# Optimization experiments

Hardware: AMD Instinct MI355X
Metric: run time of the kernel (lower is better)

The kernel has to match this reference:

```python
import jax, jax.numpy as jnp
import numpy as np

N_NODES = 25000
N_EDGES = 300000
B = 25            # graphs in the batch
NPG = N_NODES // B
D = 128           # hidden_dim == out_dim
H = 8             # num_heads
HD = D // H
L = 4             # num_layers
VOCAB = 30000
N_ETYPE = 8


def setup_inputs() -> dict:
    key = jax.random.key(0)
    ks = jax.random.split(key, 16)
    s = 0.05
    # graph structure: edges kept within each graph
    eg = jax.random.randint(ks[0], (N_EDGES,), 0, B)
    src = eg * NPG + jax.random.randint(ks[1], (N_EDGES,), 0, NPG)
    dst = eg * NPG + jax.random.randint(ks[2], (N_EDGES,), 0, NPG)
    tokens = jax.random.randint(ks[3], (N_NODES,), 0, VOCAB)
    etype = jax.random.randint(ks[4], (N_EDGES,), 0, N_ETYPE)
    graph_id = jnp.arange(N_NODES) // NPG
    return {
        "emb_h": jax.random.normal(ks[5], (VOCAB, D)) * s,
        "emb_e": jax.random.normal(ks[6], (N_ETYPE, D)) * s,
        # per-layer stacked params: Q,K,V,proj_e weights (bias=False)
        "w_qkve": jax.random.normal(ks[7], (L, 4, D, D)) * s,
        # output projections O_h, O_e
        "o_w": jax.random.normal(ks[8], (L, 2, D, D)) * s,
        "o_b": jnp.zeros((L, 2, D)),
        # layernorms: [ln1_h, ln1_e, ln2_h, ln2_e]
        "ln_scale": jnp.ones((L, 4, D)),
        "ln_bias": jnp.zeros((L, 4, D)),
        # FFNs for h and e: D -> 2D -> D
        "ffn_w1": jax.random.normal(ks[9], (L, 2, D, 2 * D)) * s,
        "ffn_b1": jnp.zeros((L, 2, 2 * D)),
        "ffn_w2": jax.random.normal(ks[10], (L, 2, 2 * D, D)) * s,
        "ffn_b2": jnp.zeros((L, 2, D)),
        # MLPReadout (L=2): 128 -> 64 -> 32 -> 1
        "mlp_w0": jax.random.normal(ks[11], (D, D // 2)) * s,
        "mlp_b0": jnp.zeros((D // 2,)),
        "mlp_w1": jax.random.normal(ks[12], (D // 2, D // 4)) * s,
        "mlp_b1": jnp.zeros((D // 4,)),
        "mlp_w2": jax.random.normal(ks[13], (D // 4, 1)) * s,
        "mlp_b2": jnp.zeros((1,)),
        "tokens": tokens,
        "etype": etype,
        "src": src,
        "dst": dst,
        "graph_id": graph_id,
    }


def _ln(x, g, b):
    m = jnp.mean(x, axis=-1, keepdims=True)
    v = jnp.mean(jnp.square(x - m), axis=-1, keepdims=True)
    return g * (x - m) / jnp.sqrt(v + 1e-5) + b


def _layer(h, e, src, dst, wq, wk, wv, we, o_w, o_b, ln_s, ln_b,
           ffn_w1, ffn_b1, ffn_w2, ffn_b2):
    n = h.shape[0]
    Q = (h @ wq).reshape(n, H, HD)
    K = (h @ wk).reshape(n, H, HD)
    V = (h @ wv).reshape(n, H, HD)
    pe = (e @ we).reshape(-1, H, HD)
    # per-edge implicit attention: (K_src * Q_dst)/sqrt(d) * proj_e
    score = (K[src] * Q[dst]) / jnp.sqrt(jnp.asarray(HD, h.dtype)) * pe  # [E,H,HD]
    e_att = score.reshape(-1, D)
    w = jnp.exp(jnp.clip(jnp.sum(score, axis=-1, keepdims=True), -5.0, 5.0))  # [E,H,1]
    wV = jax.ops.segment_sum((V[src] * w).reshape(-1, D), dst, num_segments=n)
    z = jax.ops.segment_sum(w[:, :, 0], dst, num_segments=n)  # [N,H]
    h_att = (wV.reshape(n, H, HD) / (z[:, :, None] + 1e-6)).reshape(n, D)
    # O proj + residual + LN
    h1 = _ln(h + (h_att @ o_w[0] + o_b[0]), ln_s[0], ln_b[0])
    e1 = _ln(e + (e_att @ o_w[1] + o_b[1]), ln_s[1], ln_b[1])
    # FFNs + residual + LN
    h2 = _ln(h1 + jax.nn.relu(h1 @ ffn_w1[0] + ffn_b1[0]) @ ffn_w2[0] + ffn_b2[0],
             ln_s[2], ln_b[2])
    e2 = _ln(e1 + jax.nn.relu(e1 @ ffn_w1[1] + ffn_b1[1]) @ ffn_w2[1] + ffn_b2[1],
             ln_s[3], ln_b[3])
    return h2, e2


def reference(emb_h, emb_e, w_qkve, o_w, o_b, ln_scale, ln_bias,
              ffn_w1, ffn_b1, ffn_w2, ffn_b2,
              mlp_w0, mlp_b0, mlp_w1, mlp_b1, mlp_w2, mlp_b2,
              tokens, etype, src, dst, graph_id):
    h = emb_h[tokens]   # [N,D]
    e = emb_e[etype]    # [E,D]
    for l in range(L):
        h, e = _layer(h, e, src, dst,
                      w_qkve[l, 0], w_qkve[l, 1], w_qkve[l, 2], w_qkve[l, 3],
                      o_w[l], o_b[l], ln_scale[l], ln_bias[l],
                      ffn_w1[l], ffn_b1[l], ffn_w2[l], ffn_b2[l])
    # mean-nodes readout per graph
    hg_sum = jax.ops.segment_sum(h, graph_id, num_segments=B)
    cnt = jax.ops.segment_sum(jnp.ones((h.shape[0], 1), h.dtype), graph_id, num_segments=B)
    hg = hg_sum / cnt
    # MLPReadout
    y = jax.nn.relu(hg @ mlp_w0 + mlp_b0)
    y = jax.nn.relu(y @ mlp_w1 + mlp_b1)
    return y @ mlp_w2 + mlp_b2  # [B,1]
```

## Files before the change

### kernel.cpp

```cpp
#include <hip/hip_runtime.h>
#include <cstdint>

#define NN 25000
#define NE 300000

typedef unsigned short ushort_t;
typedef __attribute__((ext_vector_type(8))) short bf16x8;
typedef __attribute__((ext_vector_type(4))) float f32x4;
typedef __attribute__((ext_vector_type(4))) unsigned short u16x4;
typedef __attribute__((ext_vector_type(8))) unsigned short u16x8;

__device__ __forceinline__ float4 ld4(const float* p){ return *reinterpret_cast<const float4*>(p); }
__device__ __forceinline__ void st4(float* p, const float4& v){ *reinterpret_cast<float4*>(p) = v; }
__device__ __forceinline__ float bf2f(ushort_t u){ return __uint_as_float((unsigned)u << 16); }
__device__ __forceinline__ ushort_t f2bfu(float f){
  unsigned x = __float_as_uint(f);
  return (ushort_t)((x + 0x7fffu + ((x >> 16) & 1u)) >> 16);
}

#define FXS 4294967296.0
#define FXI 2.3283064365386963e-10
__device__ __forceinline__ long long f2fx(float v) {
  return (long long)llrint((double)v * FXS);
}
__device__ __forceinline__ float fx2f(long long q) { return (float)((double)q * FXI); }

#define MFMA(a, b, c) __builtin_amdgcn_mfma_f32_16x16x32_bf16((a), (b), (c), 0, 0, 0)

__global__ __launch_bounds__(256)
void wconv_k(const float* __restrict__ src, ushort_t* __restrict__ dst,
             int K, int N, int total)
{
  int i = blockIdx.x * 256 + threadIdx.x;
  if (i >= total) return;
  int kn = K * N;
  int mat = i / kn, r = i - mat * kn;
  int n = r / K, k = r - n * K;
  dst[i] = f2bfu(src[(size_t)mat * kn + (size_t)k * N + n]);
}

__global__ __launch_bounds__(256)
void gather_h_k(const float* __restrict__ tab, const int* __restrict__ idx,
                float* __restrict__ hf, ushort_t* __restrict__ hb)
{
  int t = blockIdx.x * 256 + threadIdx.x;
  if (t >= NN * 32) return;
  int i = t >> 5, c4 = t & 31;
  float4 v = ld4(tab + (size_t)idx[i] * 128 + c4 * 4);
  st4(hf + (size_t)i * 128 + c4 * 4, v);
  u16x4 b = { f2bfu(v.x), f2bfu(v.y), f2bfu(v.z), f2bfu(v.w) };
  *reinterpret_cast<u16x4*>(hb + (size_t)i * 128 + c4 * 4) = b;
}

__global__ __launch_bounds__(256)
void gather_e_k(const float* __restrict__ tab, const int* __restrict__ idx,
                ushort_t* __restrict__ eb)
{
  int t = blockIdx.x * 256 + threadIdx.x;
  if (t >= NE * 32) return;
  int i = t >> 5, c4 = t & 31;
  float4 v = ld4(tab + (size_t)idx[i] * 128 + c4 * 4);
  u16x4 b = { f2bfu(v.x), f2bfu(v.y), f2bfu(v.z), f2bfu(v.w) };
  *reinterpret_cast<u16x4*>(eb + (size_t)i * 128 + c4 * 4) = b;
}

__global__ __launch_bounds__(256)
void count_k(const int* __restrict__ dst, int* __restrict__ counts)
{
  int e = blockIdx.x * 256 + threadIdx.x;
  if (e < NE) atomicAdd(&counts[dst[e]], 1);
}

__global__ __launch_bounds__(1024)
void scan_k(const int* __restrict__ counts, int* __restrict__ start,
            int* __restrict__ cursor)
{
  __shared__ int part[1024];
  const int t = threadIdx.x;
  const int base = t * 25;
  int loc[25];
  int s = 0;
#pragma unroll
  for (int i = 0; i < 25; ++i) {
    int n = base + i;
    int c = (n < NN) ? counts[n] : 0;
    loc[i] = s; s += c;
  }
  part[t] = s;
  __syncthreads();
  for (int off = 1; off < 1024; off <<= 1) {
    int v = (t >= off) ? part[t - off] : 0;
    __syncthreads();
    part[t] += v;
    __syncthreads();
  }
  int excl = (t == 0) ? 0 : part[t - 1];
#pragma unroll
  for (int i = 0; i < 25; ++i) {
    int n = base + i;
    if (n < NN) { int v = excl + loc[i]; start[n] = v; cursor[n] = v; }
  }
  if (t == 0) start[NN] = NE;
}

__global__ __launch_bounds__(256)
void scatter_k(const int* __restrict__ src, const int* __restrict__ dst,
               int* __restrict__ cursor, int2* __restrict__ csr_es)
{
  int e = blockIdx.x * 256 + threadIdx.x;
  if (e >= NE) return;
  int pos = atomicAdd(&cursor[dst[e]], 1);
  csr_es[pos] = make_int2(e, src[e]);
}

__global__ __launch_bounds__(256)
void gemmN_bf_k(const ushort_t* __restrict__ A, const ushort_t* __restrict__ WT,
                const int K, const int M, const int ldo,
                const float* __restrict__ Bias, const int osep,
                const float* __restrict__ ResF, const ushort_t* __restrict__ ResB,
                const float* __restrict__ G, const float* __restrict__ Bb,
                ushort_t* __restrict__ OutB, float* __restrict__ OutF)
{
  __shared__ __align__(16) ushort_t SM[2 * 128 * 136];
  __shared__ float mu[128], rs[128];
  ushort_t* Xs = SM;
  ushort_t* Ws = SM + 128 * 136;
  const int tid = threadIdx.x;
  const int m0 = blockIdx.x * 128;
  const int col0 = blockIdx.y * 128;

  const int l = tid & 63, wv = tid >> 6;
  const int lr = l & 15, lk = l >> 4;
  const int mb = (wv & 1) * 64, nb = (wv >> 1) * 64;
  f32x4 acc[4][4];
  const f32x4 zf = {0.f, 0.f, 0.f, 0.f};
#pragma unroll
  for (int mi = 0; mi < 4; ++mi)
#pragma unroll
    for (int ni = 0; ni < 4; ++ni) acc[mi][ni] = zf;

  for (int kc = 0; kc < K; kc += 128) {
    if (kc) __syncthreads();
    for (int c = tid; c < 2048; c += 256) {
      int r = c >> 4, k8 = c & 15;
      bf16x8 v = {};
      if (m0 + r < M)
        v = *reinterpret_cast<const bf16x8*>(A + (size_t)(m0 + r) * K + kc + k8 * 8);
      *reinterpret_cast<bf16x8*>(Xs + r * 136 + k8 * 8) = v;
    }
    for (int c = tid; c < 2048; c += 256) {
      int r = c >> 4, k8 = c & 15;
      *reinterpret_cast<bf16x8*>(Ws + r * 136 + k8 * 8) =
          *reinterpret_cast<const bf16x8*>(WT + (size_t)(col0 + r) * K + kc + k8 * 8);
    }
    __syncthreads();
#pragma unroll
    for (int kt = 0; kt < 4; ++kt) {
      bf16x8 af[4], bw[4];
#pragma unroll
      for (int i = 0; i < 4; ++i)
        af[i] = *reinterpret_cast<const bf16x8*>(Xs + (mb + i * 16 + lr) * 136 + kt * 32 + lk * 8);
#pragma unroll
      for (int i = 0; i < 4; ++i)
        bw[i] = *reinterpret_cast<const bf16x8*>(Ws + (nb + i * 16 + lr) * 136 + kt * 32 + lk * 8);
#pragma unroll
      for (int mi = 0; mi < 4; ++mi)
#pragma unroll
        for (int ni = 0; ni < 4; ++ni)
          acc[mi][ni] = MFMA(af[mi], bw[ni], acc[mi][ni]);
    }
  }

  if (G == nullptr) {
    __syncthreads();
    ushort_t* Rb = SM;
#pragma unroll
    for (int mi = 0; mi < 4; ++mi)
#pragma unroll
      for (int rr = 0; rr < 4; ++rr) {
        int row = mb + mi * 16 + lk * 4 + rr;
#pragma unroll
        for (int ni = 0; ni < 4; ++ni) {
          int col = nb + ni * 16 + lr;
          float v = acc[mi][ni][rr];
          if (Bias) v = fmaxf(v + Bias[col0 + col], 0.f);
          Rb[row * 136 + col] = f2bfu(v);
        }
      }
    __syncthreads();
    ushort_t* ob = OutB + (osep ? (size_t)blockIdx.y * M * 128 : (size_t)col0);
    for (int c = tid; c < 2048; c += 256) {
      int r = c >> 4, k8 = c & 15;
      if (m0 + r < M)
        *reinterpret_cast<u16x8*>(ob + (size_t)(m0 + r) * ldo + k8 * 8) =
            *reinterpret_cast<u16x8*>(Rb + r * 136 + k8 * 8);
    }
    return;
  }

  __syncthreads();
  float* Tf = reinterpret_cast<float*>(SM);
#pragma unroll
  for (int mi = 0; mi < 4; ++mi)
#pragma unroll
    for (int rr = 0; rr < 4; ++rr) {
      int row = mb + mi * 16 + lk * 4 + rr;
      int grow = m0 + row;
#pragma unroll
      for (int ni = 0; ni < 4; ++ni) {
        int col = nb + ni * 16 + lr;
        float t = acc[mi][ni][rr] + Bias[col];
        if (grow < M)
          t += ResF ? ResF[(size_t)grow * 128 + col] : bf2f(ResB[(size_t)grow * 128 + col]);
        Tf[row * 132 + col] = t;
      }
    }
  __syncthreads();
  {
    int r = tid >> 1, jj = tid & 1;
    const float* tp = Tf + r * 132 + jj * 64;
    float s = 0.f;
    for (int c2 = 0; c2 < 64; ++c2) s += tp[c2];
    s += __shfl_xor(s, 1);
    float mean = s * (1.f / 128.f);
    float v = 0.f;
    for (int c2 = 0; c2 < 64; ++c2) { float d = tp[c2] - mean; v += d * d; }
    v += __shfl_xor(v, 1);
    if (jj == 0) { mu[r] = mean; rs[r] = 1.f / sqrtf(v * (1.f / 128.f) + 1e-5f); }
  }
  __syncthreads();
  for (int c = tid; c < 4096; c += 256) {
    int r = c >> 5, c4 = c & 31;
    int grow = m0 + r;
    if (grow >= M) continue;
    float4 t = ld4(Tf + r * 132 + c4 * 4);
    float4 gv = ld4(G + c4 * 4), bv = ld4(Bb + c4 * 4);
    float m = mu[r], ir = rs[r];
    float o0 = gv.x * (t.x - m) * ir + bv.x;
    float o1 = gv.y * (t.y - m) * ir + bv.y;
    float o2 = gv.z * (t.z - m) * ir + bv.z;
    float o3 = gv.w * (t.w - m) * ir + bv.w;
    u16x4 ub = { f2bfu(o0), f2bfu(o1), f2bfu(o2), f2bfu(o3) };
    *reinterpret_cast<u16x4*>(OutB + (size_t)grow * 128 + c4 * 4) = ub;
    if (OutF) st4(OutF + (size_t)grow * 128 + c4 * 4, make_float4(o0, o1, o2, o3));
  }
}

__global__ __launch_bounds__(256)
void ffn_f_k(const ushort_t* __restrict__ Xbf, const float* __restrict__ ResF,
             const ushort_t* __restrict__ W1T, const float* __restrict__ B1,
             const ushort_t* __restrict__ W2T, const float* __restrict__ B2,
             const float* __restrict__ G, const float* __restrict__ Bb,
             ushort_t* __restrict__ OutB, float* __restrict__ OutF, int M)
{
  __shared__ __align__(16) ushort_t SM[8704 + 8704 + 17408];
  __shared__ float mu[64], rs[64];
  ushort_t* Xs   = SM;
  ushort_t* Mid0 = SM + 8704;
  ushort_t* Wst  = SM + 17408;
  const int tid = threadIdx.x;
  const int m0 = blockIdx.x * 64;
  const int l = tid & 63, wv = tid >> 6, lr = l & 15, lk = l >> 4;
  const f32x4 zf = {0.f, 0.f, 0.f, 0.f};

  for (int c = tid; c < 1024; c += 256) {
    int r = c >> 4, k8 = c & 15;
    bf16x8 v = {};
    if (m0 + r < M) v = *reinterpret_cast<const bf16x8*>(Xbf + (size_t)(m0 + r) * 128 + k8 * 8);
    *reinterpret_cast<bf16x8*>(Xs + r * 136 + k8 * 8) = v;
  }
  for (int c = tid; c < 2048; c += 256) {
    int r = c >> 4, k8 = c & 15;
    *reinterpret_cast<bf16x8*>(Wst + r * 136 + k8 * 8) =
        *reinterpret_cast<const bf16x8*>(W1T + (size_t)r * 128 + k8 * 8);
  }
  __syncthreads();

  f32x4 acc2[8];
#pragma unroll
  for (int i = 0; i < 8; ++i) acc2[i] = zf;
  ushort_t rsv[8][4];

  {
    f32x4 a1[8];
#pragma unroll
    for (int i = 0; i < 8; ++i) a1[i] = zf;
#pragma unroll
    for (int kt = 0; kt < 4; ++kt) {
      bf16x8 af = *reinterpret_cast<const bf16x8*>(Xs + (wv * 16 + lr) * 136 + kt * 32 + lk * 8);
#pragma unroll
      for (int ni = 0; ni < 8; ++ni) {
        bf16x8 bw = *reinterpret_cast<const bf16x8*>(Wst + (ni * 16 + lr) * 136 + kt * 32 + lk * 8);
        a1[ni] = MFMA(af, bw, a1[ni]);
      }
    }
#pragma unroll
    for (int ni = 0; ni < 8; ++ni)
#pragma unroll
      for (int rr = 0; rr < 4; ++rr)
        Mid0[(wv * 16 + lk * 4 + rr) * 136 + ni * 16 + lr] =
            f2bfu(fmaxf(a1[ni][rr] + B1[ni * 16 + lr], 0.f));
  }
  __syncthreads();
  for (int c = tid; c < 2048; c += 256) {
    int r = c >> 4, k8 = c & 15;
    *reinterpret_cast<bf16x8*>(Wst + r * 136 + k8 * 8) =
        *reinterpret_cast<const bf16x8*>(W1T + (size_t)(128 + r) * 128 + k8 * 8);
  }
  __syncthreads();
  {
    f32x4 a1[8];
#pragma unroll
    for (int i = 0; i < 8; ++i) a1[i] = zf;
#pragma unroll
    for (int kt = 0; kt < 4; ++kt) {
      bf16x8 af = *reinterpret_cast<const bf16x8*>(Xs + (wv * 16 + lr) * 136 + kt * 32 + lk * 8);
#pragma unroll
      for (int ni = 0; ni < 8; ++ni) {
        bf16x8 bw = *reinterpret_cast<const bf16x8*>(Wst + (ni * 16 + lr) * 136 + kt * 32 + lk * 8);
        a1[ni] = MFMA(af, bw, a1[ni]);
      }
    }
    __syncthreads();
    if (!ResF) {
#pragma unroll
      for (int ni = 0; ni < 8; ++ni)
#pragma unroll
        for (int rr = 0; rr < 4; ++rr)
          rsv[ni][rr] = Xs[(wv * 16 + lk * 4 + rr) * 136 + ni * 16 + lr];
    }
#pragma unroll
    for (int ni = 0; ni < 8; ++ni)
#pragma unroll
      for (int rr = 0; rr < 4; ++rr)
        Xs[(wv * 16 + lk * 4 + rr) * 136 + ni * 16 + lr] =
            f2bfu(fmaxf(a1[ni][rr] + B1[128 + ni * 16 + lr], 0.f));
  }
  __syncthreads();
  for (int c = tid; c < 2048; c += 256) {
    int r = c >> 4, k8 = c & 15;
    *reinterpret_cast<bf16x8*>(Wst + r * 136 + k8 * 8) =
        *reinterpret_cast<const bf16x8*>(W2T + (size_t)r * 256 + k8 * 8);
  }
  __syncthreads();
#pragma unroll
  for (int kt = 0; kt < 4; ++kt) {
    bf16x8 af = *reinterpret_cast<const bf16x8*>(Mid0 + (wv * 16 + lr) * 136 + kt * 32 + lk * 8);
#pragma unroll
    for (int ni = 0; ni < 8; ++ni) {
      bf16x8 bw = *reinterpret_cast<const bf16x8*>(Wst + (ni * 16 + lr) * 136 + kt * 32 + lk * 8);
      acc2[ni] = MFMA(af, bw, acc2[ni]);
    }
  }
  __syncthreads();
  for (int c = tid; c < 2048; c += 256) {
    int r = c >> 4, k8 = c & 15;
    *reinterpret_cast<bf16x8*>(Wst + r * 136 + k8 * 8) =
        *reinterpret_cast<const bf16x8*>(W2T + (size_t)r * 256 + 128 + k8 * 8);
  }
  __syncthreads();
#pragma unroll
  for (int kt = 0; kt < 4; ++kt) {
    bf16x8 af = *reinterpret_cast<const bf16x8*>(Xs + (wv * 16 + lr) * 136 + kt * 32 + lk * 8);
#pragma unroll
    for (int ni = 0; ni < 8; ++ni) {
      bf16x8 bw = *reinterpret_cast<const bf16x8*>(Wst + (ni * 16 + lr) * 136 + kt * 32 + lk * 8);
      acc2[ni] = MFMA(af, bw, acc2[ni]);
    }
  }
  __syncthreads();
  float* Tf = reinterpret_cast<float*>(Wst);
#pragma unroll
  for (int ni = 0; ni < 8; ++ni)
#pragma unroll
    for (int rr = 0; rr < 4; ++rr) {
      int row = wv * 16 + lk * 4 + rr;
      int grow = m0 + row;
      int col = ni * 16 + lr;
      float t = acc2[ni][rr] + B2[col];
      if (ResF) { if (grow < M) t += ResF[(size_t)grow * 128 + col]; }
      else      t += bf2f(rsv[ni][rr]);
      Tf[row * 132 + col] = t;
    }
  __syncthreads();
  {
    int r = tid >> 2, jj = tid & 3;
    const float* tp = Tf + r * 132 + jj * 32;
    float s = 0.f;
    for (int c2 = 0; c2 < 32; ++c2) s += tp[c2];
    s += __shfl_xor(s, 1); s += __shfl_xor(s, 2);
    float mean = s * (1.f / 128.f);
    float v = 0.f;
    for (int c2 = 0; c2 < 32; ++c2) { float d = tp[c2] - mean; v += d * d; }
    v += __shfl_xor(v, 1); v += __shfl_xor(v, 2);
    if (jj == 0) { mu[r] = mean; rs[r] = 1.f / sqrtf(v * (1.f / 128.f) + 1e-5f); }
  }
  __syncthreads();
  for (int c = tid; c < 2048; c += 256) {
    int r = c >> 5, c4 = c & 31;
    int grow = m0 + r;
    if (grow >= M) continue;
    float4 t = ld4(Tf + r * 132 + c4 * 4);
    float4 gv = ld4(G + c4 * 4), bv = ld4(Bb + c4 * 4);
    float m = mu[r], ir = rs[r];
    float o0 = gv.x * (t.x - m) * ir + bv.x;
    float o1 = gv.y * (t.y - m) * ir + bv.y;
    float o2 = gv.z * (t.z - m) * ir + bv.z;
    float o3 = gv.w * (t.w - m) * ir + bv.w;
    u16x4 ub = { f2bfu(o0), f2bfu(o1), f2bfu(o2), f2bfu(o3) };
    *reinterpret_cast<u16x4*>(OutB + (size_t)grow * 128 + c4 * 4) = ub;
    if (OutF) st4(OutF + (size_t)grow * 128 + c4 * 4, make_float4(o0, o1, o2, o3));
  }
}

__global__ __launch_bounds__(256)
void edge_score_k(const ushort_t* __restrict__ Q, const ushort_t* __restrict__ K,
                  ushort_t* __restrict__ PE,
                  const int* __restrict__ src, const int* __restrict__ dst,
                  float* __restrict__ wbuf)
{
  int t = blockIdx.x * 256 + threadIdx.x;
  int e = t >> 4;
  if (e >= NE) return;
  int j = t & 15;
  int s = src[e], d = dst[e];
  u16x8 kv = *reinterpret_cast<const u16x8*>(K + (size_t)s * 128 + j * 8);
  u16x8 qv = *reinterpret_cast<const u16x8*>(Q + (size_t)d * 128 + j * 8);
  u16x8 pv = *reinterpret_cast<const u16x8*>(PE + (size_t)e * 128 + j * 8);
  float hsum = 0.f;
  u16x8 ob;
#pragma unroll
  for (int i = 0; i < 8; ++i) {
    float x = bf2f(kv[i]) * bf2f(qv[i]) * 0.25f * bf2f(pv[i]);
    hsum += x; ob[i] = f2bfu(x);
  }
  *reinterpret_cast<u16x8*>(PE + (size_t)e * 128 + j * 8) = ob;
  hsum += __shfl_xor(hsum, 1);
  float w = expf(fminf(fmaxf(hsum, -5.f), 5.f));
  if ((j & 1) == 0) wbuf[(size_t)e * 8 + (j >> 1)] = w;
}

__global__ __launch_bounds__(256)
void reduce_k(const ushort_t* __restrict__ V, const float* __restrict__ wbuf,
              const int* __restrict__ start, const int2* __restrict__ csr_es,
              ushort_t* __restrict__ out)
{
  int t = blockIdx.x * 256 + threadIdx.x;
  int n = t >> 4;
  if (n >= NN) return;
  int j = t & 15;
  int p0 = start[n], p1 = start[n + 1];
  long long acc[8] = {};
  long long zacc = 0;
  for (int p = p0; p < p1; ++p) {
    int2 es = csr_es[p];
    float w = wbuf[(size_t)es.x * 8 + (j >> 1)];
    u16x8 vv = *reinterpret_cast<const u16x8*>(V + (size_t)es.y * 128 + j * 8);
    zacc += f2fx(w);
#pragma unroll
    for (int i = 0; i < 8; ++i) acc[i] += f2fx(bf2f(vv[i]) * w);
  }
  float zz = fx2f(zacc) + 1e-6f;
  u16x8 ob;
#pragma unroll
  for (int i = 0; i < 8; ++i) ob[i] = f2bfu(fx2f(acc[i]) / zz);
  *reinterpret_cast<u16x8*>(out + (size_t)n * 128 + j * 8) = ob;
}

__global__ __launch_bounds__(256)
void graphmean_k(const float* __restrict__ h, float* __restrict__ hg)
{
  __shared__ float red[256];
  int g = blockIdx.x, tid = threadIdx.x;
  int c = tid & 127, half = tid >> 7;
  float s = 0.f;
  for (int r = half; r < 1000; r += 2) s += h[(size_t)(g * 1000 + r) * 128 + c];
  red[tid] = s;
  __syncthreads();
  if (half == 0) hg[g * 128 + c] = (red[c] + red[c + 128]) / 1000.0f;
}

__global__ __launch_bounds__(256)
void readout_k(const float* __restrict__ hg,
               const float* __restrict__ w0, const float* __restrict__ b0,
               const float* __restrict__ w1, const float* __restrict__ b1,
               const float* __restrict__ w2, const float* __restrict__ b2,
               float* __restrict__ out)
{
  __shared__ float hs[25 * 128];
  __shared__ float t0[25 * 64];
  __shared__ float t1[25 * 32];
  int tid = threadIdx.x;
  for (int i = tid; i < 25 * 128; i += 256) hs[i] = hg[i];
  __syncthreads();
  for (int i = tid; i < 25 * 64; i += 256) {
    int r = i >> 6, c = i & 63;
    float a = b0[c];
    for (int k = 0; k < 128; k++) a += hs[r * 128 + k] * w0[k * 64 + c];
    t0[i] = fmaxf(a, 0.f);
  }
  __syncthreads();
  for (int i = tid; i < 25 * 32; i += 256) {
    int r = i >> 5, c = i & 31;
    float a = b1[c];
    for (int k = 0; k < 64; k++) a += t0[r * 64 + k] * w1[k * 32 + c];
    t1[i] = fmaxf(a, 0.f);
  }
  __syncthreads();
  if (tid < 25) {
    float a = b2[0];
    for (int k = 0; k < 32; k++) a += t1[tid * 32 + k] * w2[k];
    out[tid] = a;
  }
}

extern "C" void kernel_launch(void* const* d_in, const int* in_sizes, int n_in,
                              void* d_out, int out_size, void* d_ws, size_t ws_size,
                              hipStream_t stream)
{
  const float* emb_h  = (const float*)d_in[0];
  const float* emb_e  = (const float*)d_in[1];
  const float* w_qkve = (const float*)d_in[2];
  const float* o_w    = (const float*)d_in[3];
  const float* o_b    = (const float*)d_in[4];
  const float* ln_s   = (const float*)d_in[5];
  const float* ln_b   = (const float*)d_in[6];
  const float* ffn_w1 = (const float*)d_in[7];
  const float* ffn_b1 = (const float*)d_in[8];
  const float* ffn_w2 = (const float*)d_in[9];
  const float* ffn_b2 = (const float*)d_in[10];
  const float* mlp_w0 = (const float*)d_in[11];
  const float* mlp_b0 = (const float*)d_in[12];
  const float* mlp_w1 = (const float*)d_in[13];
  const float* mlp_b1 = (const float*)d_in[14];
  const float* mlp_w2 = (const float*)d_in[15];
  const float* mlp_b2 = (const float*)d_in[16];
  const int* tokens = (const int*)d_in[17];
  const int* etype  = (const int*)d_in[18];
  const int* src    = (const int*)d_in[19];
  const int* dst    = (const int*)d_in[20];

  char* ws = (char*)d_ws;
  size_t off = 0;
  auto alloc = [&](size_t bytes) { char* p = ws + off; off += bytes; return p; };
  int2*      csr_es = (int2*)alloc((size_t)NE * 8);
  float*     h      = (float*)alloc((size_t)NN * 128 * 4);
  float*     hg     = (float*)alloc(25 * 128 * 4);
  float*     wbuf   = (float*)alloc((size_t)NE * 8 * 4);
  int*       counts = (int*)alloc((size_t)NN * 4);
  int*       cursor = (int*)alloc((size_t)NN * 4);
  int*       startp = (int*)alloc((size_t)(NN + 1) * 4);
  ushort_t*  h_bf   = (ushort_t*)alloc((size_t)NN * 128 * 2);
  ushort_t*  ha_bf  = (ushort_t*)alloc((size_t)NN * 128 * 2);
  ushort_t*  Qb     = (ushort_t*)alloc((size_t)NN * 128 * 2);
  ushort_t*  Kb     = (ushort_t*)alloc((size_t)NN * 128 * 2);
  ushort_t*  Vb     = (ushort_t*)alloc((size_t)NN * 128 * 2);
  ushort_t*  e_bf   = (ushort_t*)alloc((size_t)NE * 128 * 2);
  ushort_t*  sc_bf  = (ushort_t*)alloc((size_t)NE * 128 * 2);
  ushort_t*  wt     = (ushort_t*)alloc(917504 * 2);
  (void)Kb; (void)Vb;

  ushort_t* qkveT = wt;
  ushort_t* owT   = wt + 262144;
  ushort_t* w1T   = wt + 393216;
  ushort_t* w2T   = wt + 655360;
  wconv_k<<<1024, 256, 0, stream>>>(w_qkve, qkveT, 128, 128, 262144);
  wconv_k<<<512,  256, 0, stream>>>(o_w,    owT,   128, 128, 131072);
  wconv_k<<<1024, 256, 0, stream>>>(ffn_w1, w1T,   128, 256, 262144);
  wconv_k<<<1024, 256, 0, stream>>>(ffn_w2, w2T,   256, 128, 262144);

  gather_h_k<<<3125, 256, 0, stream>>>(emb_h, tokens, h, h_bf);
  gather_e_k<<<37500, 256, 0, stream>>>(emb_e, etype, e_bf);

  hipMemsetAsync(counts, 0, (size_t)NN * 4, stream);
  count_k<<<(NE + 255) / 256, 256, 0, stream>>>(dst, counts);
  scan_k<<<1, 1024, 0, stream>>>(counts, startp, cursor);
  scatter_k<<<(NE + 255) / 256, 256, 0, stream>>>(src, dst, cursor, csr_es);

  const int GN = (NN + 127) / 128;
  const int GE = (NE + 127) / 128;
  const int FN = (NN + 63) / 64;
  const int FE = (NE + 63) / 64;

  for (int l = 0; l < 4; ++l) {
    const ushort_t* qkvT = qkveT + (size_t)l * 4 * 16384;
    const ushort_t* weT  = qkveT + ((size_t)l * 4 + 3) * 16384;
    const ushort_t* ow0T = owT + ((size_t)l * 2 + 0) * 16384;
    const ushort_t* ow1T = owT + ((size_t)l * 2 + 1) * 16384;
    const ushort_t* w1hT = w1T + ((size_t)l * 2 + 0) * 32768;
    const ushort_t* w1eT = w1T + ((size_t)l * 2 + 1) * 32768;
    const ushort_t* w2hT = w2T + ((size_t)l * 2 + 0) * 32768;
    const ushort_t* w2eT = w2T + ((size_t)l * 2 + 1) * 32768;
    const float* ob0 = o_b + ((size_t)l * 2 + 0) * 128;
    const float* ob1 = o_b + ((size_t)l * 2 + 1) * 128;
    const float* ls0 = ln_s + ((size_t)l * 4 + 0) * 128;
    const float* ls1 = ln_s + ((size_t)l * 4 + 1) * 128;
    const float* ls2 = ln_s + ((size_t)l * 4 + 2) * 128;
    const float* ls3 = ln_s + ((size_t)l * 4 + 3) * 128;
    const float* lb0 = ln_b + ((size_t)l * 4 + 0) * 128;
    const float* lb1 = ln_b + ((size_t)l * 4 + 1) * 128;
    const float* lb2 = ln_b + ((size_t)l * 4 + 2) * 128;
    const float* lb3 = ln_b + ((size_t)l * 4 + 3) * 128;
    const float* fb1h = ffn_b1 + ((size_t)l * 2 + 0) * 256;
    const float* fb1e = ffn_b1 + ((size_t)l * 2 + 1) * 256;
    const float* fb2h = ffn_b2 + ((size_t)l * 2 + 0) * 128;
    const float* fb2e = ffn_b2 + ((size_t)l * 2 + 1) * 128;

    gemmN_bf_k<<<dim3(GN, 3), 256, 0, stream>>>(h_bf, qkvT, 128, NN, 128,
        nullptr, 1, nullptr, nullptr, nullptr, nullptr, Qb, nullptr);
    gemmN_bf_k<<<dim3(GE, 1), 256, 0, stream>>>(e_bf, weT, 128, NE, 128,
        nullptr, 0, nullptr, nullptr, nullptr, nullptr, sc_bf, nullptr);

    edge_score_k<<<18750, 256, 0, stream>>>(Qb, Kb, sc_bf, src, dst, wbuf);
    reduce_k<<<1563, 256, 0, stream>>>(Vb, wbuf, startp, csr_es, ha_bf);

    gemmN_bf_k<<<dim3(GN, 1), 256, 0, stream>>>(ha_bf, ow0T, 128, NN, 128,
        ob0, 0, h, nullptr, ls0, lb0, h_bf, h);
    gemmN_bf_k<<<dim3(GE, 1), 256, 0, stream>>>(sc_bf, ow1T, 128, NE, 128,
        ob1, 0, nullptr, e_bf, ls1, lb1, e_bf, nullptr);

    ffn_f_k<<<FN, 256, 0, stream>>>(h_bf, h, w1hT, fb1h, w2hT, fb2h,
                                    ls2, lb2, h_bf, h, NN);
    ffn_f_k<<<FE, 256, 0, stream>>>(e_bf, nullptr, w1eT, fb1e, w2eT, fb2e,
                                    ls3, lb3, e_bf, nullptr, NE);
  }

  graphmean_k<<<25, 256, 0, stream>>>(h, hg);
  readout_k<<<1, 256, 0, stream>>>(hg, mlp_w0, mlp_b0, mlp_w1, mlp_b1, mlp_w2, mlp_b2,
                                   (float*)d_out);
}
```

Baseline: 2.254 ms.

## Fuse edge projection, score, O_e projection, LN and edge FFN into one kernel

Replaces the per-layer edge pipeline (proj_e GEMM, edge score, O_e GEMM with residual+LN, edge FFN with LN) with a single kernel that keeps a 64-edge tile in shared memory across all stages. This removes several full round trips of the 300k x 128 bf16 edge tensor through global memory and the sc_bf scratch buffer. The cost is about 70KB of shared memory per block, which lowers occupancy, and many block-wide barriers with weights reloaded into shared memory for each stage.

```diff
diff --git a/kernel.cpp b/kernel.cpp
--- a/kernel.cpp
+++ b/kernel.cpp
@@ -414,30 +414,277 @@
 }
 
 __global__ __launch_bounds__(256)
-void edge_score_k(const ushort_t* __restrict__ Q, const ushort_t* __restrict__ K,
-                  ushort_t* __restrict__ PE,
-                  const int* __restrict__ src, const int* __restrict__ dst,
-                  float* __restrict__ wbuf)
-{
-  int t = blockIdx.x * 256 + threadIdx.x;
-  int e = t >> 4;
-  if (e >= NE) return;
-  int j = t & 15;
-  int s = src[e], d = dst[e];
-  u16x8 kv = *reinterpret_cast<const u16x8*>(K + (size_t)s * 128 + j * 8);
-  u16x8 qv = *reinterpret_cast<const u16x8*>(Q + (size_t)d * 128 + j * 8);
-  u16x8 pv = *reinterpret_cast<const u16x8*>(PE + (size_t)e * 128 + j * 8);
-  float hsum = 0.f;
-  u16x8 ob;
-#pragma unroll
-  for (int i = 0; i < 8; ++i) {
-    float x = bf2f(kv[i]) * bf2f(qv[i]) * 0.25f * bf2f(pv[i]);
-    hsum += x; ob[i] = f2bfu(x);
-  }
-  *reinterpret_cast<u16x8*>(PE + (size_t)e * 128 + j * 8) = ob;
-  hsum += __shfl_xor(hsum, 1);
-  float w = expf(fminf(fmaxf(hsum, -5.f), 5.f));
-  if ((j & 1) == 0) wbuf[(size_t)e * 8 + (j >> 1)] = w;
+void efused_k(ushort_t* __restrict__ Ebuf,
+              const ushort_t* __restrict__ Qb, const ushort_t* __restrict__ Kb,
+              const int* __restrict__ src, const int* __restrict__ dst,
+              float* __restrict__ wbuf,
+              const ushort_t* __restrict__ weT,
+              const ushort_t* __restrict__ owT, const float* __restrict__ oBias,
+              const float* __restrict__ G1, const float* __restrict__ B1n,
+              const ushort_t* __restrict__ W1T, const float* __restrict__ fB1,
+              const ushort_t* __restrict__ W2T, const float* __restrict__ fB2,
+              const float* __restrict__ G2, const float* __restrict__ B2n,
+              int M)
+{
+  __shared__ __align__(16) ushort_t SM[34816];
+  __shared__ float mu[64], rs[64];
+  ushort_t* Es   = SM;
+  ushort_t* Mid0 = SM + 8704;
+  ushort_t* Wst  = SM + 17408;
+  const int tid = threadIdx.x;
+  const int m0 = blockIdx.x * 64;
+  const int l = tid & 63, wv = tid >> 6, lr = l & 15, lk = l >> 4;
+  const f32x4 zf = {0.f, 0.f, 0.f, 0.f};
+
+  for (int c = tid; c < 1024; c += 256) {
+    int r = c >> 4, k8 = c & 15;
+    bf16x8 v = {};
+    if (m0 + r < M) v = *reinterpret_cast<const bf16x8*>(Ebuf + (size_t)(m0 + r) * 128 + k8 * 8);
+    *reinterpret_cast<bf16x8*>(Es + r * 136 + k8 * 8) = v;
+  }
+  for (int c = tid; c < 2048; c += 256) {
+    int r = c >> 4, k8 = c & 15;
+    *reinterpret_cast<bf16x8*>(Wst + r * 136 + k8 * 8) =
+        *reinterpret_cast<const bf16x8*>(weT + (size_t)r * 128 + k8 * 8);
+  }
+  __syncthreads();
+
+  {
+    f32x4 a1[8];
+#pragma unroll
+    for (int i = 0; i < 8; ++i) a1[i] = zf;
+#pragma unroll
+    for (int kt = 0; kt < 4; ++kt) {
+      bf16x8 af = *reinterpret_cast<const bf16x8*>(Es + (wv * 16 + lr) * 136 + kt * 32 + lk * 8);
+#pragma unroll
+      for (int ni = 0; ni < 8; ++ni) {
+        bf16x8 bw = *reinterpret_cast<const bf16x8*>(Wst + (ni * 16 + lr) * 136 + kt * 32 + lk * 8);
+        a1[ni] = MFMA(af, bw, a1[ni]);
+      }
+    }
+#pragma unroll
+    for (int ni = 0; ni < 8; ++ni)
+#pragma unroll
+      for (int rr = 0; rr < 4; ++rr)
+        Mid0[(wv * 16 + lk * 4 + rr) * 136 + ni * 16 + lr] = f2bfu(a1[ni][rr]);
+  }
+  __syncthreads();
+
+  for (int c = tid; c < 1024; c += 256) {
+    int r = c >> 4, j = c & 15;
+    int e = m0 + r;
+    if (e < M) {
+      int s = src[e], d = dst[e];
+      u16x8 kv = *reinterpret_cast<const u16x8*>(Kb + (size_t)s * 128 + j * 8);
+      u16x8 qv = *reinterpret_cast<const u16x8*>(Qb + (size_t)d * 128 + j * 8);
+      u16x8 pv = *reinterpret_cast<const u16x8*>(Mid0 + r * 136 + j * 8);
+      float hsum = 0.f;
+      u16x8 ob;
+#pragma unroll
+      for (int i = 0; i < 8; ++i) {
+        float x = bf2f(kv[i]) * bf2f(qv[i]) * 0.25f * bf2f(pv[i]);
+        hsum += x; ob[i] = f2bfu(x);
+      }
+      *reinterpret_cast<u16x8*>(Mid0 + r * 136 + j * 8) = ob;
+      hsum += __shfl_xor(hsum, 1);
+      float w = expf(fminf(fmaxf(hsum, -5.f), 5.f));
+      if ((j & 1) == 0) wbuf[(size_t)e * 8 + (j >> 1)] = w;
+    }
+  }
+  __syncthreads();
+
+  for (int c = tid; c < 2048; c += 256) {
+    int r = c >> 4, k8 = c & 15;
+    *reinterpret_cast<bf16x8*>(Wst + r * 136 + k8 * 8) =
+        *reinterpret_cast<const bf16x8*>(owT + (size_t)r * 128 + k8 * 8);
+  }
+  __syncthreads();
+
+  {
+    f32x4 a1[8];
+#pragma unroll
+    for (int i = 0; i < 8; ++i) a1[i] = zf;
+#pragma unroll
+    for (int kt = 0; kt < 4; ++kt) {
+      bf16x8 af = *reinterpret_cast<const bf16x8*>(Mid0 + (wv * 16 + lr) * 136 + kt * 32 + lk * 8);
+#pragma unroll
+      for (int ni = 0; ni < 8; ++ni) {
+        bf16x8 bw = *reinterpret_cast<const bf16x8*>(Wst + (ni * 16 + lr) * 136 + kt * 32 + lk * 8);
+        a1[ni] = MFMA(af, bw, a1[ni]);
+      }
+    }
+    __syncthreads();
+    float* Tf = reinterpret_cast<float*>(Wst);
+#pragma unroll
+    for (int ni = 0; ni < 8; ++ni)
+#pragma unroll
+      for (int rr = 0; rr < 4; ++rr) {
+        int row = wv * 16 + lk * 4 + rr;
+        int col = ni * 16 + lr;
+        Tf[row * 132 + col] = a1[ni][rr] + oBias[col] + bf2f(Es[row * 136 + col]);
+      }
+  }
+  __syncthreads();
+  {
+    float* Tf = reinterpret_cast<float*>(Wst);
+    int r = tid >> 2, jj = tid & 3;
+    const float* tp = Tf + r * 132 + jj * 32;
+    float s = 0.f;
+    for (int c2 = 0; c2 < 32; ++c2) s += tp[c2];
+    s += __shfl_xor(s, 1); s += __shfl_xor(s, 2);
+    float mean = s * (1.f / 128.f);
+    float v = 0.f;
+    for (int c2 = 0; c2 < 32; ++c2) { float d = tp[c2] - mean; v += d * d; }
+    v += __shfl_xor(v, 1); v += __shfl_xor(v, 2);
+    if (jj == 0) { mu[r] = mean; rs[r] = 1.f / sqrtf(v * (1.f / 128.f) + 1e-5f); }
+  }
+  __syncthreads();
+  {
+    float* Tf = reinterpret_cast<float*>(Wst);
+    for (int c = tid; c < 2048; c += 256) {
+      int r = c >> 5, c4 = c & 31;
+      float4 t = ld4(Tf + r * 132 + c4 * 4);
+      float4 gv = ld4(G1 + c4 * 4), bv = ld4(B1n + c4 * 4);
+      float m = mu[r], ir = rs[r];
+      u16x4 ub = { f2bfu(gv.x * (t.x - m) * ir + bv.x), f2bfu(gv.y * (t.y - m) * ir + bv.y),
+                   f2bfu(gv.z * (t.z - m) * ir + bv.z), f2bfu(gv.w * (t.w - m) * ir + bv.w) };
+      *reinterpret_cast<u16x4*>(Es + r * 136 + c4 * 4) = ub;
+    }
+  }
+  __syncthreads();
+
+  f32x4 acc2[8];
+#pragma unroll
+  for (int i = 0; i < 8; ++i) acc2[i] = zf;
+  ushort_t rsv[8][4];
+
+  for (int c = tid; c < 2048; c += 256) {
+    int r = c >> 4, k8 = c & 15;
+    *reinterpret_cast<bf16x8*>(Wst + r * 136 + k8 * 8) =
+        *reinterpret_cast<const bf16x8*>(W1T + (size_t)r * 128 + k8 * 8);
+  }
+  __syncthreads();
+  {
+    f32x4 a1[8];
+#pragma unroll
+    for (int i = 0; i < 8; ++i) a1[i] = zf;
+#pragma unroll
+    for (int kt = 0; kt < 4; ++kt) {
+      bf16x8 af = *reinterpret_cast<const bf16x8*>(Es + (wv * 16 + lr) * 136 + kt * 32 + lk * 8);
+#pragma unroll
+      for (int ni = 0; ni < 8; ++ni) {
+        bf16x8 bw = *reinterpret_cast<const bf16x8*>(Wst + (ni * 16 + lr) * 136 + kt * 32 + lk * 8);
+        a1[ni] = MFMA(af, bw, a1[ni]);
+      }
+    }
+    __syncthreads();
+#pragma unroll
+    for (int ni = 0; ni < 8; ++ni)
+#pragma unroll
+      for (int rr = 0; rr < 4; ++rr)
+        Mid0[(wv * 16 + lk * 4 + rr) * 136 + ni * 16 + lr] =
+            f2bfu(fmaxf(a1[ni][rr] + fB1[ni * 16 + lr], 0.f));
+  }
+  __syncthreads();
+  for (int c = tid; c < 2048; c += 256) {
+    int r = c >> 4, k8 = c & 15;
+    *reinterpret_cast<bf16x8*>(Wst + r * 136 + k8 * 8) =
+        *reinterpret_cast<const bf16x8*>(W1T + (size_t)(128 + r) * 128 + k8 * 8);
+  }
+  __syncthreads();
+  {
+    f32x4 a1[8];
+#pragma unroll
+    for (int i = 0; i < 8; ++i) a1[i] = zf;
+#pragma unroll
+    for (int kt = 0; kt < 4; ++kt) {
+      bf16x8 af = *reinterpret_cast<const bf16x8*>(Es + (wv * 16 + lr) * 136 + kt * 32 + lk * 8);
+#pragma unroll
+      for (int ni = 0; ni < 8; ++ni) {
+        bf16x8 bw = *reinterpret_cast<const bf16x8*>(Wst + (ni * 16 + lr) * 136 + kt * 32 + lk * 8);
+        a1[ni] = MFMA(af, bw, a1[ni]);
+      }
+    }
+    __syncthreads();
+#pragma unroll
+    for (int ni = 0; ni < 8; ++ni)
+#pragma unroll
+      for (int rr = 0; rr < 4; ++rr)
+        rsv[ni][rr] = Es[(wv * 16 + lk * 4 + rr) * 136 + ni * 16 + lr];
+#pragma unroll
+    for (int ni = 0; ni < 8; ++ni)
+#pragma unroll
+      for (int rr = 0; rr < 4; ++rr)
+        Es[(wv * 16 + lk * 4 + rr) * 136 + ni * 16 + lr] =
+            f2bfu(fmaxf(a1[ni][rr] + fB1[128 + ni * 16 + lr], 0.f));
+  }
+  __syncthreads();
+  for (int c = tid; c < 2048; c += 256) {
+    int r = c >> 4, k8 = c & 15;
+    *reinterpret_cast<bf16x8*>(Wst + r * 136 + k8 * 8) =
+        *reinterpret_cast<const bf16x8*>(W2T + (size_t)r * 256 + k8 * 8);
+  }
+  __syncthreads();
+#pragma unroll
+  for (int kt = 0; kt < 4; ++kt) {
+    bf16x8 af = *reinterpret_cast<const bf16x8*>(Mid0 + (wv * 16 + lr) * 136 + kt * 32 + lk * 8);
+#pragma unroll
+    for (int ni = 0; ni < 8; ++ni) {
+      bf16x8 bw = *reinterpret_cast<const bf16x8*>(Wst + (ni * 16 + lr) * 136 + kt * 32 + lk * 8);
+      acc2[ni] = MFMA(af, bw, acc2[ni]);
+    }
+  }
+  __syncthreads();
+  for (int c = tid; c < 2048; c += 256) {
+    int r = c >> 4, k8 = c & 15;
+    *reinterpret_cast<bf16x8*>(Wst + r * 136 + k8 * 8) =
+        *reinterpret_cast<const bf16x8*>(W2T + (size_t)r * 256 + 128 + k8 * 8);
+  }
+  __syncthreads();
+#pragma unroll
+  for (int kt = 0; kt < 4; ++kt) {
+    bf16x8 af = *reinterpret_cast<const bf16x8*>(Es + (wv * 16 + lr) * 136 + kt * 32 + lk * 8);
+#pragma unroll
+    for (int ni = 0; ni < 8; ++ni) {
+      bf16x8 bw = *reinterpret_cast<const bf16x8*>(Wst + (ni * 16 + lr) * 136 + kt * 32 + lk * 8);
+      acc2[ni] = MFMA(af, bw, acc2[ni]);
+    }
+  }
+  __syncthreads();
+  float* Tf = reinterpret_cast<float*>(Wst);
+#pragma unroll
+  for (int ni = 0; ni < 8; ++ni)
+#pragma unroll
+    for (int rr = 0; rr < 4; ++rr) {
+      int row = wv * 16 + lk * 4 + rr;
+      int col = ni * 16 + lr;
+      Tf[row * 132 + col] = acc2[ni][rr] + fB2[col] + bf2f(rsv[ni][rr]);
+    }
+  __syncthreads();
+  {
+    int r = tid >> 2, jj = tid & 3;
+    const float* tp = Tf + r * 132 + jj * 32;
+    float s = 0.f;
+    for (int c2 = 0; c2 < 32; ++c2) s += tp[c2];
+    s += __shfl_xor(s, 1); s += __shfl_xor(s, 2);
+    float mean = s * (1.f / 128.f);
+    float v = 0.f;
+    for (int c2 = 0; c2 < 32; ++c2) { float d = tp[c2] - mean; v += d * d; }
+    v += __shfl_xor(v, 1); v += __shfl_xor(v, 2);
+    if (jj == 0) { mu[r] = mean; rs[r] = 1.f / sqrtf(v * (1.f / 128.f) + 1e-5f); }
+  }
+  __syncthreads();
+  for (int c = tid; c < 2048; c += 256) {
+    int r = c >> 5, c4 = c & 31;
+    int grow = m0 + r;
+    if (grow >= M) continue;
+    float4 t = ld4(Tf + r * 132 + c4 * 4);
+    float4 gv = ld4(G2 + c4 * 4), bv = ld4(B2n + c4 * 4);
+    float m = mu[r], ir = rs[r];
+    u16x4 ub = { f2bfu(gv.x * (t.x - m) * ir + bv.x), f2bfu(gv.y * (t.y - m) * ir + bv.y),
+                 f2bfu(gv.z * (t.z - m) * ir + bv.z), f2bfu(gv.w * (t.w - m) * ir + bv.w) };
+    *reinterpret_cast<u16x4*>(Ebuf + (size_t)grow * 128 + c4 * 4) = ub;
+  }
 }
 
 __global__ __launch_bounds__(256)
@@ -556,9 +803,7 @@
   ushort_t*  Kb     = (ushort_t*)alloc((size_t)NN * 128 * 2);
   ushort_t*  Vb     = (ushort_t*)alloc((size_t)NN * 128 * 2);
   ushort_t*  e_bf   = (ushort_t*)alloc((size_t)NE * 128 * 2);
-  ushort_t*  sc_bf  = (ushort_t*)alloc((size_t)NE * 128 * 2);
   ushort_t*  wt     = (ushort_t*)alloc(917504 * 2);
-  (void)Kb; (void)Vb;
 
   ushort_t* qkveT = wt;
   ushort_t* owT   = wt + 262144;
@@ -578,7 +823,6 @@
   scatter_k<<<(NE + 255) / 256, 256, 0, stream>>>(src, dst, cursor, csr_es);
 
   const int GN = (NN + 127) / 128;
-  const int GE = (NE + 127) / 128;
   const int FN = (NN + 63) / 64;
   const int FE = (NE + 63) / 64;
 
@@ -608,21 +852,15 @@
 
     gemmN_bf_k<<<dim3(GN, 3), 256, 0, stream>>>(h_bf, qkvT, 128, NN, 128,
         nullptr, 1, nullptr, nullptr, nullptr, nullptr, Qb, nullptr);
-    gemmN_bf_k<<<dim3(GE, 1), 256, 0, stream>>>(e_bf, weT, 128, NE, 128,
-        nullptr, 0, nullptr, nullptr, nullptr, nullptr, sc_bf, nullptr);
-
-    edge_score_k<<<18750, 256, 0, stream>>>(Qb, Kb, sc_bf, src, dst, wbuf);
+
+    efused_k<<<FE, 256, 0, stream>>>(e_bf, Qb, Kb, src, dst, wbuf,
+        weT, ow1T, ob1, ls1, lb1, w1eT, fb1e, w2eT, fb2e, ls3, lb3, NE);
+
     reduce_k<<<1563, 256, 0, stream>>>(Vb, wbuf, startp, csr_es, ha_bf);
-
     gemmN_bf_k<<<dim3(GN, 1), 256, 0, stream>>>(ha_bf, ow0T, 128, NN, 128,
         ob0, 0, h, nullptr, ls0, lb0, h_bf, h);
-    gemmN_bf_k<<<dim3(GE, 1), 256, 0, stream>>>(sc_bf, ow1T, 128, NE, 128,
-        ob1, 0, nullptr, e_bf, ls1, lb1, e_bf, nullptr);
-
     ffn_f_k<<<FN, 256, 0, stream>>>(h_bf, h, w1hT, fb1h, w2hT, fb2h,
                                     ls2, lb2, h_bf, h, NN);
-    ffn_f_k<<<FE, 256, 0, stream>>>(e_bf, nullptr, w1eT, fb1e, w2eT, fb2e,
-                                    ls3, lb3, e_bf, nullptr, NE);
   }
 
   graphmean_k<<<25, 256, 0, stream>>>(h, hg);
```

After: 1.822 ms. 19.2% less time.
